# Kernel tuning notes

Hardware: AMD Instinct MI355X
Metric: run time of the kernel (lower is better)

Reference implementation:

```python
import jax, jax.numpy as jnp
import numpy as np

NHRZ, BATCH, NU, NY, NH = 2048, 128, 64, 64, 256  # NH even; half-size rotation params


def setup_inputs() -> dict:
    key = jax.random.key(0)
    ks = jax.random.split(key, 9)
    H = NH // 2
    damping = 0.9  # dampingConstantInitial < 1.0
    return {
        "y0": jax.random.normal(ks[0], (BATCH, NY), jnp.float32),
        "U": jax.random.normal(ks[1], (NHRZ, BATCH, NU), jnp.float32),
        # torch init: lmbd_cont_real = -log(damping) * ones(H); imag ~ U[0,1)
        "lmbd_cont_real": jnp.full((H,), -np.log(damping), jnp.float32),
        "lmbd_cont_imag": jax.random.uniform(ks[2], (H,), jnp.float32),
        "B": jax.random.normal(ks[3], (NH, NU), jnp.float32) / np.sqrt(NU),
        "Wy2x": jax.random.normal(ks[4], (NH, NY), jnp.float32) / np.sqrt(NY),
        "by2x": jax.random.normal(ks[5], (NH,), jnp.float32) * 0.01,
        "Wx2y": jax.random.normal(ks[6], (NY, NH), jnp.float32) / np.sqrt(NH),
        "bx2y": jax.random.normal(ks[7], (NY,), jnp.float32) * 0.01,
    }


def reference(y0, U, lmbd_cont_real, lmbd_cont_imag, B, Wy2x, by2x, Wx2y, bx2y):
    H = lmbd_cont_real.shape[0]  # Nhidden // 2
    r = jnp.exp(-jnp.abs(lmbd_cont_real))
    theta = (np.pi / 2) * lmbd_cont_imag
    lr = r * jnp.cos(theta)   # [H]
    li = r * jnp.sin(theta)   # [H]
    nf = jnp.sqrt(1.0 - jnp.exp(-2.0 * jnp.abs(lmbd_cont_real)))
    nf2 = jnp.concatenate((nf, nf))                       # [2H]
    Bu = jnp.einsum('tbu,hu->tbh', U, B) * nf2            # [T, B, 2H]
    x0 = y0 @ Wy2x.T + by2x                               # [B, 2H]

    # A = [[diag(lr), -diag(li)], [diag(li), diag(lr)]]; x_new = x @ A.T = A x
    def step(x, bu):
        x1, x2 = x[..., :H], x[..., H:]
        xn = jnp.concatenate((lr * x1 - li * x2, li * x1 + lr * x2), axis=-1) + bu
        return xn, xn

    _, Xs = jax.lax.scan(step, x0, Bu)                    # [T, B, 2H]
    X = jnp.concatenate((x0[None], Xs), axis=0)           # [T+1, B, 2H]
    Y = X @ Wx2y.T + bx2y                                 # [T+1, B, Ny]
    return Y
```

## Files before the change

### kernel.cpp

```cpp
#include <hip/hip_runtime.h>
#include <hip/hip_bf16.h>

typedef __bf16 bf16x8 __attribute__((ext_vector_type(8)));
typedef float  f32x4  __attribute__((ext_vector_type(4)));

constexpr int kNHRZ = 2048, kBATCH = 128, kNU = 64, kNY = 64, kNH = 256, kH = 128;
constexpr int kCHUNK = 256, kNCHUNK = kNHRZ / kCHUNK;
constexpr int kTS = 16, kBT = 2, kM = kTS * kBT;
constexpr int kNSUB = kCHUNK / kTS;

constexpr int U_STR  = 72;
constexpr int BU_STR = 272;
constexpr int X_STR  = 264;

constexpr int OFF_U  = 0;
constexpr int OFF_BU = OFF_U + kM * U_STR * 2;
constexpr int OFF_X  = OFF_BU + kM * BU_STR * 2;
constexpr int SMEM1  = OFF_X;
constexpr int SMEM2  = OFF_X + kM * X_STR * 2;

__device__ inline bf16x8 pack8(float4 a, float4 b) {
    bf16x8 v;
    v[0] = (__bf16)a.x; v[1] = (__bf16)a.y; v[2] = (__bf16)a.z; v[3] = (__bf16)a.w;
    v[4] = (__bf16)b.x; v[5] = (__bf16)b.y; v[6] = (__bf16)b.z; v[7] = (__bf16)b.w;
    return v;
}

template <bool FINAL>
__global__ __launch_bounds__(256, 2) void scan_mfma(
    const float* __restrict__ U,
    const float* __restrict__ lre,
    const float* __restrict__ lim,
    const float* __restrict__ Bmat,
    const float* __restrict__ Wx2y,
    const float* __restrict__ bx2y,
    const float* __restrict__ starts,
    float* __restrict__ ends,
    float* __restrict__ out)
{
    extern __shared__ char smem[];
    __bf16* Us = (__bf16*)(smem + OFF_U);
    __bf16* Bu = (__bf16*)(smem + OFF_BU);
    __bf16* Xs = (__bf16*)(smem + OFF_X);

    const int tid  = threadIdx.x;
    const int lane = tid & 63;
    const int w    = tid >> 6;
    const int lw   = lane & 15;
    const int lg   = lane >> 4;
    const int blk  = blockIdx.x;
    const int c    = blk >> 6;
    const int bp   = blk & 63;
    const int bglob = bp * 2;
    const int t0   = c * kCHUNK;

    bf16x8 Bf[2][4];
#pragma unroll
    for (int nt = 0; nt < 4; ++nt) {
        const int h  = w * 64 + nt * 16 + lw;
        const float ab = fabsf(lre[h & (kH - 1)]);
        const float nf = sqrtf(fmaxf(0.0f, 1.0f - expf(-2.0f * ab)));
#pragma unroll
        for (int ks = 0; ks < 2; ++ks) {
            const float* p = Bmat + h * kNU + ks * 32 + lg * 8;
            float4 f0 = ((const float4*)p)[0];
            float4 f1 = ((const float4*)p)[1];
            f0.x *= nf; f0.y *= nf; f0.z *= nf; f0.w *= nf;
            f1.x *= nf; f1.y *= nf; f1.z *= nf; f1.w *= nf;
            Bf[ks][nt] = pack8(f0, f1);
        }
    }

    bf16x8 Wf[8][2];
    float  bias[2] = {0.f, 0.f};
    if constexpr (FINAL) {
#pragma unroll
        for (int nt = 0; nt < 2; ++nt) {
            const int y = (w >> 1) * 32 + nt * 16 + lw;
            bias[nt] = bx2y[y];
#pragma unroll
            for (int ks = 0; ks < 8; ++ks) {
                const float* p = Wx2y + y * kNH + ks * 32 + lg * 8;
                Wf[ks][nt] = pack8(((const float4*)p)[0], ((const float4*)p)[1]);
            }
        }
    }

    const int hm = tid & 127;
    const int bl = tid >> 7;
    float lr, li;
    {
        const float ab = fabsf(lre[hm]);
        const float r  = expf(-ab);
        const float th = 1.5707963267948966f * lim[hm];
        lr = r * cosf(th);
        li = r * sinf(th);
    }
    float x1, x2;
    if constexpr (FINAL) {
        const size_t sb = ((size_t)c * kBATCH + bglob + bl) * kNH;
        x1 = starts[sb + hm];
        x2 = starts[sb + hm + kH];
    } else {
        x1 = 0.0f; x2 = 0.0f;
    }

    const int sm = tid >> 3, sq = tid & 7;
    const float* uptr0 =
        U + ((size_t)(t0 + (sm >> 1)) * kBATCH + (bglob + (sm & 1))) * kNU + sq * 8;

    float4 u0 = ((const float4*)uptr0)[0];
    float4 u1 = ((const float4*)uptr0)[1];

#pragma unroll 1
    for (int s = 0; s < kNSUB; ++s) {
        *(bf16x8*)&Us[sm * U_STR + sq * 8] = pack8(u0, u1);
        if (s + 1 < kNSUB) {
            const float* p = uptr0 + (size_t)(s + 1) * kTS * kBATCH * kNU;
            u0 = ((const float4*)p)[0];
            u1 = ((const float4*)p)[1];
        }
        __syncthreads();

        {
            f32x4 acc[2][4] = {};
#pragma unroll
            for (int ks = 0; ks < 2; ++ks) {
                bf16x8 a0 = *(const bf16x8*)&Us[(lw)      * U_STR + ks * 32 + lg * 8];
                bf16x8 a1 = *(const bf16x8*)&Us[(16 + lw) * U_STR + ks * 32 + lg * 8];
#pragma unroll
                for (int nt = 0; nt < 4; ++nt) {
                    acc[0][nt] = __builtin_amdgcn_mfma_f32_16x16x32_bf16(a0, Bf[ks][nt], acc[0][nt], 0, 0, 0);
                    acc[1][nt] = __builtin_amdgcn_mfma_f32_16x16x32_bf16(a1, Bf[ks][nt], acc[1][nt], 0, 0, 0);
                }
            }
#pragma unroll
            for (int mt = 0; mt < 2; ++mt)
#pragma unroll
                for (int nt = 0; nt < 4; ++nt)
#pragma unroll
                    for (int i = 0; i < 4; ++i)
                        Bu[(mt * 16 + lg * 4 + i) * BU_STR + w * 64 + nt * 16 + lw] =
                            (__bf16)acc[mt][nt][i];
        }
        __syncthreads();

#pragma unroll
        for (int t = 0; t < kTS; ++t) {
            const int m = t * kBT + bl;
            const float bu1 = (float)Bu[m * BU_STR + hm];
            const float bu2 = (float)Bu[m * BU_STR + kH + hm];
            const float n1 = fmaf(lr, x1, fmaf(-li, x2, bu1));
            const float n2 = fmaf(li, x1, fmaf(lr, x2, bu2));
            x1 = n1; x2 = n2;
            if constexpr (FINAL) {
                Xs[m * X_STR + hm]      = (__bf16)x1;
                Xs[m * X_STR + kH + hm] = (__bf16)x2;
            }
        }

        if constexpr (FINAL) {
            __syncthreads();
            f32x4 acc[2] = {};
            const int mt = w & 1;
#pragma unroll
            for (int ks = 0; ks < 8; ++ks) {
                bf16x8 a = *(const bf16x8*)&Xs[(mt * 16 + lw) * X_STR + ks * 32 + lg * 8];
                acc[0] = __builtin_amdgcn_mfma_f32_16x16x32_bf16(a, Wf[ks][0], acc[0], 0, 0, 0);
                acc[1] = __builtin_amdgcn_mfma_f32_16x16x32_bf16(a, Wf[ks][1], acc[1], 0, 0, 0);
            }
#pragma unroll
            for (int i = 0; i < 4; ++i) {
                const int m = mt * 16 + lg * 4 + i;
                const int t = t0 + s * kTS + (m >> 1);
                const int b = bglob + (m & 1);
                float* orow = out + ((size_t)(1 + t) * kBATCH + b) * kNY + (w >> 1) * 32 + lw;
#pragma unroll
                for (int nt = 0; nt < 2; ++nt)
                    orow[nt * 16] = acc[nt][i] + bias[nt];
            }
        }
    }

    if constexpr (!FINAL) {
        const size_t eb = ((size_t)c * kBATCH + bglob + bl) * kNH;
        ends[eb + hm]      = x1;
        ends[eb + hm + kH] = x2;
    }
}

__global__ __launch_bounds__(128) void combine_kernel(
    const float* __restrict__ y0, const float* __restrict__ Wy2x,
    const float* __restrict__ by2x, const float* __restrict__ lre,
    const float* __restrict__ lim, const float* __restrict__ ends,
    float* __restrict__ starts)
{
    const int b  = blockIdx.x;
    const int hm = threadIdx.x;

    const float ab = fabsf(lre[hm]);
    const float r  = expf(-ab);
    const float th = 1.5707963267948966f * lim[hm];
    float lr = r * cosf(th);
    float li = r * sinf(th);
    float pr = lr, pi = li;
#pragma unroll
    for (int k = 0; k < 8; ++k) {
        const float nr = pr * pr - pi * pi;
        const float ni = 2.0f * pr * pi;
        pr = nr; pi = ni;
    }

    float s1 = by2x[hm];
    float s2 = by2x[hm + kH];
#pragma unroll 8
    for (int q = 0; q < kNY; ++q) {
        const float yv = y0[b * kNY + q];
        s1 = fmaf(Wy2x[hm * kNY + q], yv, s1);
        s2 = fmaf(Wy2x[(hm + kH) * kNY + q], yv, s2);
    }

    for (int c = 0; c < kNCHUNK; ++c) {
        const size_t base = ((size_t)c * kBATCH + b) * kNH;
        starts[base + hm]      = s1;
        starts[base + hm + kH] = s2;
        const float e1 = ends[base + hm];
        const float e2 = ends[base + hm + kH];
        const float n1 = fmaf(pr, s1, fmaf(-pi, s2, e1));
        const float n2 = fmaf(pi, s1, fmaf(pr, s2, e2));
        s1 = n1; s2 = n2;
    }
}

__global__ __launch_bounds__(64) void y0_kernel(
    const float* __restrict__ starts, const float* __restrict__ Wx2y,
    const float* __restrict__ bx2y, float* __restrict__ out)
{
    const int b = blockIdx.x;
    const int y = threadIdx.x;
    const float* x0 = starts + (size_t)b * kNH;
    float acc = bx2y[y];
#pragma unroll 4
    for (int h = 0; h < kNH; h += 4) {
        float4 xv = *(const float4*)&x0[h];
        float4 wv = *(const float4*)&Wx2y[y * kNH + h];
        acc = fmaf(wv.x, xv.x, acc);
        acc = fmaf(wv.y, xv.y, acc);
        acc = fmaf(wv.z, xv.z, acc);
        acc = fmaf(wv.w, xv.w, acc);
    }
    out[(size_t)b * kNY + y] = acc;
}

extern "C" void kernel_launch(void* const* d_in, const int* in_sizes, int n_in,
                              void* d_out, int out_size, void* d_ws, size_t ws_size,
                              hipStream_t stream) {
    const float* y0   = (const float*)d_in[0];
    const float* U    = (const float*)d_in[1];
    const float* lre  = (const float*)d_in[2];
    const float* lim  = (const float*)d_in[3];
    const float* Bmat = (const float*)d_in[4];
    const float* Wy2x = (const float*)d_in[5];
    const float* by2x = (const float*)d_in[6];
    const float* Wx2y = (const float*)d_in[7];
    const float* bx2y = (const float*)d_in[8];
    float* out = (float*)d_out;

    float* ends   = (float*)d_ws;
    float* starts = ends + (size_t)kNCHUNK * kBATCH * kNH;

    const int grid = kNCHUNK * (kBATCH / kBT);

    scan_mfma<false><<<grid, 256, SMEM1, stream>>>(
        U, lre, lim, Bmat, nullptr, nullptr, nullptr, ends, nullptr);
    combine_kernel<<<kBATCH, 128, 0, stream>>>(
        y0, Wy2x, by2x, lre, lim, ends, starts);
    y0_kernel<<<kBATCH, 64, 0, stream>>>(starts, Wx2y, bx2y, out);
    scan_mfma<true><<<grid, 256, SMEM2, stream>>>(
        U, lre, lim, Bmat, Wx2y, bx2y, starts, nullptr, out);
}
```

Baseline: 91.81 us.

## Double-buffer U and Bu in LDS to overlap the input GEMM with the recurrence

Double-buffers the U and Bu shared-memory tiles so the MFMA projection of the next sub-chunk's inputs is issued before the current sub-chunk's serial recurrence and stored after it. This cuts one of the two barriers per sub-chunk and lets MFMA work overlap the scalar FMA chain. The Bu row stride also changes from 272 to 260 to alter the LDS bank mapping. The cost is more LDS per block and more live accumulator registers across the recurrence, which may hurt the two-blocks-per-CU occupancy.

```diff
diff --git a/kernel.cpp b/kernel.cpp
--- a/kernel.cpp
+++ b/kernel.cpp
@@ -10,12 +10,12 @@
 constexpr int kNSUB = kCHUNK / kTS;
 
 constexpr int U_STR  = 72;
-constexpr int BU_STR = 272;
+constexpr int BU_STR = 260;
 constexpr int X_STR  = 264;
 
 constexpr int OFF_U  = 0;
-constexpr int OFF_BU = OFF_U + kM * U_STR * 2;
-constexpr int OFF_X  = OFF_BU + kM * BU_STR * 2;
+constexpr int OFF_BU = OFF_U + 2 * kM * U_STR * 2;
+constexpr int OFF_X  = OFF_BU + 2 * kM * BU_STR * 2;
 constexpr int SMEM1  = OFF_X;
 constexpr int SMEM2  = OFF_X + kM * X_STR * 2;
 
@@ -39,9 +39,9 @@
     float* __restrict__ out)
 {
     extern __shared__ char smem[];
-    __bf16* Us = (__bf16*)(smem + OFF_U);
-    __bf16* Bu = (__bf16*)(smem + OFF_BU);
-    __bf16* Xs = (__bf16*)(smem + OFF_X);
+    __bf16* UsB = (__bf16*)(smem + OFF_U);
+    __bf16* BuB = (__bf16*)(smem + OFF_BU);
+    __bf16* Xs  = (__bf16*)(smem + OFF_X);
 
     const int tid  = threadIdx.x;
     const int lane = tid & 63;
@@ -108,48 +108,66 @@
     const int sm = tid >> 3, sq = tid & 7;
     const float* uptr0 =
         U + ((size_t)(t0 + (sm >> 1)) * kBATCH + (bglob + (sm & 1))) * kNU + sq * 8;
+    const size_t ustep = (size_t)kTS * kBATCH * kNU;
+
+    auto gemm1 = [&](const __bf16* Ubuf, f32x4 (&acc)[2][4]) {
+#pragma unroll
+        for (int ks = 0; ks < 2; ++ks) {
+            bf16x8 a0 = *(const bf16x8*)&Ubuf[(lw)      * U_STR + ks * 32 + lg * 8];
+            bf16x8 a1 = *(const bf16x8*)&Ubuf[(16 + lw) * U_STR + ks * 32 + lg * 8];
+#pragma unroll
+            for (int nt = 0; nt < 4; ++nt) {
+                acc[0][nt] = __builtin_amdgcn_mfma_f32_16x16x32_bf16(a0, Bf[ks][nt], acc[0][nt], 0, 0, 0);
+                acc[1][nt] = __builtin_amdgcn_mfma_f32_16x16x32_bf16(a1, Bf[ks][nt], acc[1][nt], 0, 0, 0);
+            }
+        }
+    };
+    auto store_bu = [&](__bf16* Bubuf, const f32x4 (&acc)[2][4]) {
+#pragma unroll
+        for (int mt = 0; mt < 2; ++mt)
+#pragma unroll
+            for (int nt = 0; nt < 4; ++nt)
+#pragma unroll
+                for (int i = 0; i < 4; ++i)
+                    Bubuf[(mt * 16 + lg * 4 + i) * BU_STR + w * 64 + nt * 16 + lw] =
+                        (__bf16)acc[mt][nt][i];
+    };
 
     float4 u0 = ((const float4*)uptr0)[0];
     float4 u1 = ((const float4*)uptr0)[1];
+    *(bf16x8*)&UsB[sm * U_STR + sq * 8] = pack8(u0, u1);
+    u0 = ((const float4*)(uptr0 + ustep))[0];
+    u1 = ((const float4*)(uptr0 + ustep))[1];
+    __syncthreads();
+    {
+        f32x4 acc[2][4] = {};
+        gemm1(UsB, acc);
+        store_bu(BuB, acc);
+    }
+    *(bf16x8*)&UsB[kM * U_STR + sm * U_STR + sq * 8] = pack8(u0, u1);
+    if (2 < kNSUB) {
+        u0 = ((const float4*)(uptr0 + 2 * ustep))[0];
+        u1 = ((const float4*)(uptr0 + 2 * ustep))[1];
+    }
+    __syncthreads();
 
 #pragma unroll 1
     for (int s = 0; s < kNSUB; ++s) {
-        *(bf16x8*)&Us[sm * U_STR + sq * 8] = pack8(u0, u1);
-        if (s + 1 < kNSUB) {
-            const float* p = uptr0 + (size_t)(s + 1) * kTS * kBATCH * kNU;
-            u0 = ((const float4*)p)[0];
-            u1 = ((const float4*)p)[1];
-        }
-        __syncthreads();
-
-        {
-            f32x4 acc[2][4] = {};
-#pragma unroll
-            for (int ks = 0; ks < 2; ++ks) {
-                bf16x8 a0 = *(const bf16x8*)&Us[(lw)      * U_STR + ks * 32 + lg * 8];
-                bf16x8 a1 = *(const bf16x8*)&Us[(16 + lw) * U_STR + ks * 32 + lg * 8];
-#pragma unroll
-                for (int nt = 0; nt < 4; ++nt) {
-                    acc[0][nt] = __builtin_amdgcn_mfma_f32_16x16x32_bf16(a0, Bf[ks][nt], acc[0][nt], 0, 0, 0);
-                    acc[1][nt] = __builtin_amdgcn_mfma_f32_16x16x32_bf16(a1, Bf[ks][nt], acc[1][nt], 0, 0, 0);
-                }
-            }
-#pragma unroll
-            for (int mt = 0; mt < 2; ++mt)
-#pragma unroll
-                for (int nt = 0; nt < 4; ++nt)
-#pragma unroll
-                    for (int i = 0; i < 4; ++i)
-                        Bu[(mt * 16 + lg * 4 + i) * BU_STR + w * 64 + nt * 16 + lw] =
-                            (__bf16)acc[mt][nt][i];
-        }
-        __syncthreads();
+        const int cur = s & 1, nxt = cur ^ 1;
+        __bf16* Buc = BuB + cur * (kM * BU_STR);
+        __bf16* Bun = BuB + nxt * (kM * BU_STR);
+        __bf16* Usn = UsB + nxt * (kM * U_STR);
+        __bf16* Usc = UsB + cur * (kM * U_STR);
+        const bool hasNext = (s + 1 < kNSUB);
+
+        f32x4 acc[2][4] = {};
+        if (hasNext) gemm1(Usn, acc);
 
 #pragma unroll
         for (int t = 0; t < kTS; ++t) {
             const int m = t * kBT + bl;
-            const float bu1 = (float)Bu[m * BU_STR + hm];
-            const float bu2 = (float)Bu[m * BU_STR + kH + hm];
+            const float bu1 = (float)Buc[m * BU_STR + hm];
+            const float bu2 = (float)Buc[m * BU_STR + kH + hm];
             const float n1 = fmaf(lr, x1, fmaf(-li, x2, bu1));
             const float n2 = fmaf(li, x1, fmaf(lr, x2, bu2));
             x1 = n1; x2 = n2;
@@ -159,15 +177,26 @@
             }
         }
 
+        if (hasNext) {
+            store_bu(Bun, acc);
+            if (s + 2 < kNSUB) {
+                *(bf16x8*)&Usc[sm * U_STR + sq * 8] = pack8(u0, u1);
+                if (s + 3 < kNSUB) {
+                    u0 = ((const float4*)(uptr0 + (size_t)(s + 3) * ustep))[0];
+                    u1 = ((const float4*)(uptr0 + (size_t)(s + 3) * ustep))[1];
+                }
+            }
+        }
+
         if constexpr (FINAL) {
             __syncthreads();
-            f32x4 acc[2] = {};
+            f32x4 acc2[2] = {};
             const int mt = w & 1;
 #pragma unroll
             for (int ks = 0; ks < 8; ++ks) {
                 bf16x8 a = *(const bf16x8*)&Xs[(mt * 16 + lw) * X_STR + ks * 32 + lg * 8];
-                acc[0] = __builtin_amdgcn_mfma_f32_16x16x32_bf16(a, Wf[ks][0], acc[0], 0, 0, 0);
-                acc[1] = __builtin_amdgcn_mfma_f32_16x16x32_bf16(a, Wf[ks][1], acc[1], 0, 0, 0);
+                acc2[0] = __builtin_amdgcn_mfma_f32_16x16x32_bf16(a, Wf[ks][0], acc2[0], 0, 0, 0);
+                acc2[1] = __builtin_amdgcn_mfma_f32_16x16x32_bf16(a, Wf[ks][1], acc2[1], 0, 0, 0);
             }
 #pragma unroll
             for (int i = 0; i < 4; ++i) {
@@ -177,8 +206,11 @@
                 float* orow = out + ((size_t)(1 + t) * kBATCH + b) * kNY + (w >> 1) * 32 + lw;
 #pragma unroll
                 for (int nt = 0; nt < 2; ++nt)
-                    orow[nt * 16] = acc[nt][i] + bias[nt];
-            }
+                    orow[nt * 16] = acc2[nt][i] + bias[nt];
+            }
+            if (hasNext) __syncthreads();
+        } else {
+            if (hasNext) __syncthreads();
         }
     }
 
```

Measured after the change: 96.89 us. 1.06x slower.
